# Performance work log

Hardware: AMD Instinct MI355X
Metric: run time of the kernel (lower is better)

The kernel has to match this reference:

```python
import jax, jax.numpy as jnp
import numpy as np

B, S, E, H = 2, 2048, 1024, 16
D = E // H  # head_dim = 64

def setup_inputs() -> dict:
    key = jax.random.key(0)
    ks = jax.random.split(key, 5)
    scale = 0.02
    return {
        "x": jax.random.normal(ks[0], (B, S, E), dtype=jnp.float32),
        "Wq": jax.random.normal(ks[1], (E, E), dtype=jnp.float32) * scale,
        "Wk": jax.random.normal(ks[2], (E, E), dtype=jnp.float32) * scale,
        "Wv": jax.random.normal(ks[3], (E, E), dtype=jnp.float32) * scale,
        "Wo": jax.random.normal(ks[4], (E, E), dtype=jnp.float32) * scale,
        "bo": jnp.zeros((E,), dtype=jnp.float32),
    }

def reference(x, Wq, Wk, Wv, Wo, bo):
    b, s, e = x.shape
    # Linear projections (torch Linear: x @ W.T), split heads -> (b, h, s, d)
    q = (x @ Wq.T).reshape(b, s, H, D).transpose(0, 2, 1, 3)
    k = (x @ Wk.T).reshape(b, s, H, D).transpose(0, 2, 1, 3)
    v = (x @ Wv.T).reshape(b, s, H, D).transpose(0, 2, 1, 3)
    # Full materialized causal scores (b, h, s, s)
    scores = jnp.einsum("bhqd,bhkd->bhqk", q, k)
    causal = jnp.tril(jnp.ones((s, s), dtype=bool))  # True = keep
    scores = jnp.where(causal, scores, -jnp.inf)
    attn = jax.nn.softmax(scores / jnp.sqrt(jnp.float32(D)), axis=-1)
    ctx = jnp.einsum("bhqk,bhkd->bhqd", attn, v)
    ctx = ctx.transpose(0, 2, 1, 3).reshape(b, s, e)
    return ctx @ Wo.T + bo
```

## Files before the change

### kernel.cpp

```cpp
#include <hip/hip_runtime.h>
#include <hip/hip_bf16.h>

typedef __attribute__((ext_vector_type(8))) short short8_t;
typedef __attribute__((ext_vector_type(4))) short s4v;
typedef __attribute__((ext_vector_type(4))) float f32x4_t;
using u16 = unsigned short;

constexpr int S_LEN = 2048;
constexpr int EMB   = 1024;
constexpr int NH    = 16;
constexpr int HD    = 64;
constexpr int BATCH = 2;
constexpr int MR    = BATCH * S_LEN;
constexpr int E3    = 3 * EMB;

#define L2E 1.44269504f

__device__ __forceinline__ u16 f2bf(float f) {
  unsigned u = __builtin_bit_cast(unsigned, f);
  unsigned r = 0x7fffu + ((u >> 16) & 1u);
  return (u16)((u + r) >> 16);
}

__device__ __forceinline__ void gld16(const void* g, void* l) {
  __builtin_amdgcn_global_load_lds(
      (const __attribute__((address_space(1))) void*)g,
      (__attribute__((address_space(3))) void*)l, 16, 0, 0);
}

template <int OFF>
__device__ __forceinline__ s4v tr16(const __attribute__((address_space(3))) u16* p) {
  s4v d;
  asm volatile("ds_read_b64_tr_b16 %0, %1 offset:%2"
               : "=v"(d) : "v"(p), "n"(OFF));
  return d;
}

__global__ void k_cvt_all(const float* __restrict__ x, const float* __restrict__ Wq,
                          const float* __restrict__ Wk, const float* __restrict__ Wv,
                          const float* __restrict__ Wo, u16* __restrict__ out) {
  int i = blockIdx.x * 256 + threadIdx.x;
  const float* src;
  int j;
  float sc = 1.0f;
  if (i < (1 << 20)) {
    src = x; j = i;
  } else {
    int jj = i - (1 << 20);
    int r = jj >> 18;
    j = jj & ((1 << 18) - 1);
    src = (r == 0) ? Wq : (r == 1) ? Wk : (r == 2) ? Wv : Wo;
    if (r == 0) sc = 0.125f;
  }
  float4 v = reinterpret_cast<const float4*>(src)[j];
  ushort4 o;
  o.x = f2bf(v.x * sc); o.y = f2bf(v.y * sc);
  o.z = f2bf(v.z * sc); o.w = f2bf(v.w * sc);
  reinterpret_cast<ushort4*>(out)[i] = o;
}

template <bool F32OUT>
__global__ __launch_bounds__(256) void k_gemm_bt(
    const u16* __restrict__ A, const u16* __restrict__ Bw,
    void* __restrict__ Cv, const float* __restrict__ bias,
    int M, int N, int K) {
  __shared__ short As[128 * 32];
  __shared__ short Bs[128 * 32];
  const int t    = threadIdx.x;
  const int w    = t >> 6;
  const int ln15 = t & 15;
  const int lg   = (t >> 4) & 3;
  const int wr   = w >> 1, wc = w & 1;
  const int m0   = blockIdx.y * 128, n0 = blockIdx.x * 128;

  const int srow = t >> 2;
  const int scol = (t & 3) * 8;
  const u16* gA = A + (size_t)(m0 + srow) * K + scol;
  const u16* gB = Bw + (size_t)(n0 + srow) * K + scol;
  short* lA = As + w * 512;
  short* lB = Bs + w * 512;

  f32x4_t acc[4][4] = {};

  for (int k0 = 0; k0 < K; k0 += 32) {
    gld16(gA + k0, lA);
    gld16(gA + (size_t)64 * K + k0, lA + 2048);
    gld16(gB + k0, lB);
    gld16(gB + (size_t)64 * K + k0, lB + 2048);
    __syncthreads();
    short8_t af[4], bf[4];
#pragma unroll
    for (int i = 0; i < 4; ++i) {
      af[i] = *reinterpret_cast<const short8_t*>(
          &As[(wr * 64 + i * 16 + ln15) * 32 + 8 * lg]);
      bf[i] = *reinterpret_cast<const short8_t*>(
          &Bs[(wc * 64 + i * 16 + ln15) * 32 + 8 * lg]);
    }
#pragma unroll
    for (int i = 0; i < 4; ++i)
#pragma unroll
      for (int j = 0; j < 4; ++j)
        acc[i][j] = __builtin_amdgcn_mfma_f32_16x16x32_bf16(
            af[i], bf[j], acc[i][j], 0, 0, 0);
    __syncthreads();
  }

  if (F32OUT) {
    float* C = reinterpret_cast<float*>(Cv);
#pragma unroll
    for (int i = 0; i < 4; ++i)
#pragma unroll
      for (int j = 0; j < 4; ++j) {
        const int col = n0 + wc * 64 + j * 16 + ln15;
        const float bv = bias ? bias[col] : 0.0f;
#pragma unroll
        for (int r = 0; r < 4; ++r) {
          const int row = m0 + wr * 64 + i * 16 + lg * 4 + r;
          C[(size_t)row * N + col] = acc[i][j][r] + bv;
        }
      }
  } else {
    u16* C = reinterpret_cast<u16*>(Cv);
#pragma unroll
    for (int i = 0; i < 4; ++i)
#pragma unroll
      for (int j = 0; j < 4; ++j) {
        const int col = n0 + wc * 64 + j * 16 + ln15;
#pragma unroll
        for (int r = 0; r < 4; ++r) {
          const int row = m0 + wr * 64 + i * 16 + lg * 4 + r;
          C[(size_t)row * N + col] = f2bf(acc[i][j][r]);
        }
      }
  }
}

__global__ __launch_bounds__(256, 4) void k_attn2(const u16* __restrict__ QKV,
                                                  u16* __restrict__ ctx) {
  __shared__ u16 Ks[2][64 * 64];
  __shared__ u16 Vs[2][64 * 64];

  const int t    = threadIdx.x;
  const int w    = t >> 6;
  const int l    = t & 63;
  const int ln15 = t & 15;
  const int lg   = (l >> 4) & 3;

  const int qt = 31 - blockIdx.y;
  const int bh = blockIdx.x;
  const int b  = bh >> 4, h = bh & 15;

  const u16* KVb = QKV + (size_t)b * S_LEN * E3 + h * HD;
  const u16* Kg  = KVb + 1024;
  const u16* Vg  = KVb + 2048;
  const int qrow = qt * 64 + w * 16;

  short8_t qf[2];
  {
    const u16* qp = KVb + (size_t)(qrow + ln15) * E3 + 8 * lg;
    qf[0] = *reinterpret_cast<const short8_t*>(qp);
    qf[1] = *reinterpret_cast<const short8_t*>(qp + 32);
  }

  const int krow_lo = l >> 3;
  const int kcol    = 8 * ((l & 7) ^ krow_lo);
  const int vkv     = l >> 1;
  const int vcol    = 16 * w + 8 * (l & 1);

  const int kx  = 8 * (ln15 & 7);
  const int kc0 = (8 * lg) ^ kx;
  const int kc1 = (32 + 8 * lg) ^ kx;

#define STAGE(buf, kv0)                                                        \
  do {                                                                         \
    gld16(Kg + (size_t)((kv0) + 16 * w + krow_lo) * E3 + kcol,                 \
          &Ks[buf][1024 * w]);                                                 \
    gld16(Kg + (size_t)((kv0) + 16 * w + 8 + krow_lo) * E3 + kcol,             \
          &Ks[buf][1024 * w + 512]);                                           \
    gld16(Vg + (size_t)((kv0) + vkv) * E3 + vcol, &Vs[buf][1024 * w]);         \
    gld16(Vg + (size_t)((kv0) + 32 + vkv) * E3 + vcol,                         \
          &Vs[buf][1024 * w + 512]);                                           \
  } while (0)

  f32x4_t o[4] = {};
  float mrow = -3e38f, lrow = 0.0f;
  const int nt_tiles = qt + 1;

  STAGE(0, 0);
  int cur = 0;

  for (int kvt = 0; kvt < nt_tiles; ++kvt) {
    const int kv0 = kvt * 64;
    asm volatile("s_barrier" ::: "memory");
    if (kvt + 1 < nt_tiles) {
      STAGE(cur ^ 1, kv0 + 64);
      asm volatile("s_waitcnt vmcnt(4)" ::: "memory");
    } else {
      asm volatile("s_waitcnt vmcnt(0)" ::: "memory");
    }
    asm volatile("s_barrier" ::: "memory");

    const __attribute__((address_space(3))) u16* vp =
        (const __attribute__((address_space(3))) u16*)&Vs[cur][4 * l];
    s4v vf[4][2][2];
#pragma unroll
    for (int nt = 0; nt < 4; ++nt) {
      if (nt == 0) { vf[0][0][0]=tr16<0>(vp);    vf[0][0][1]=tr16<512>(vp);
                     vf[0][1][0]=tr16<1024>(vp); vf[0][1][1]=tr16<1536>(vp); }
      if (nt == 1) { vf[1][0][0]=tr16<2048>(vp); vf[1][0][1]=tr16<2560>(vp);
                     vf[1][1][0]=tr16<3072>(vp); vf[1][1][1]=tr16<3584>(vp); }
      if (nt == 2) { vf[2][0][0]=tr16<4096>(vp); vf[2][0][1]=tr16<4608>(vp);
                     vf[2][1][0]=tr16<5120>(vp); vf[2][1][1]=tr16<5632>(vp); }
      if (nt == 3) { vf[3][0][0]=tr16<6144>(vp); vf[3][0][1]=tr16<6656>(vp);
                     vf[3][1][0]=tr16<7168>(vp); vf[3][1][1]=tr16<7680>(vp); }
    }

    f32x4_t tacc[4];
    __builtin_amdgcn_s_setprio(1);
#pragma unroll
    for (int ks = 0; ks < 4; ++ks) {
      const int R = 16 * ks + ln15;
      short8_t kf0 = *reinterpret_cast<const short8_t*>(&Ks[cur][R * 64 + kc0]);
      short8_t kf1 = *reinterpret_cast<const short8_t*>(&Ks[cur][R * 64 + kc1]);
      f32x4_t a = {0.f, 0.f, 0.f, 0.f};
      a = __builtin_amdgcn_mfma_f32_16x16x32_bf16(kf0, qf[0], a, 0, 0, 0);
      a = __builtin_amdgcn_mfma_f32_16x16x32_bf16(kf1, qf[1], a, 0, 0, 0);
      tacc[ks] = a;
    }
    __builtin_amdgcn_s_setprio(0);

    if (kvt == qt) {
      const int qg = qrow + ln15;
#pragma unroll
      for (int ks = 0; ks < 4; ++ks)
#pragma unroll
        for (int r = 0; r < 4; ++r)
          if (kv0 + 16 * ks + 4 * lg + r > qg) tacc[ks][r] = -3e38f;
    }

    float rm = fmaxf(
        fmaxf(fmaxf(fmaxf(tacc[0][0], tacc[0][1]), fmaxf(tacc[0][2], tacc[0][3])),
              fmaxf(fmaxf(tacc[1][0], tacc[1][1]), fmaxf(tacc[1][2], tacc[1][3]))),
        fmaxf(fmaxf(fmaxf(tacc[2][0], tacc[2][1]), fmaxf(tacc[2][2], tacc[2][3])),
              fmaxf(fmaxf(tacc[3][0], tacc[3][1]), fmaxf(tacc[3][2], tacc[3][3]))));
    rm = fmaxf(rm, __shfl_xor(rm, 16, 64));
    rm = fmaxf(rm, __shfl_xor(rm, 32, 64));

    if (__any(rm > mrow)) {
      const float nm = fmaxf(mrow, rm);
      const float sc = exp2f((mrow - nm) * L2E);
      mrow = nm;
      lrow *= sc;
#pragma unroll
      for (int r = 0; r < 4; ++r) {
        const float so = __shfl(sc, 20 * lg + r, 64);
#pragma unroll
        for (int nt = 0; nt < 4; ++nt) o[nt][r] *= so;
      }
    }

    const float nmL = mrow * L2E;
    float p[4][4];
    float rs = 0.0f;
#pragma unroll
    for (int ks = 0; ks < 4; ++ks)
#pragma unroll
      for (int r = 0; r < 4; ++r) {
        const float pv = exp2f(fmaf(tacc[ks][r], L2E, -nmL));
        p[ks][r] = pv;
        rs += pv;
      }
    rs += __shfl_xor(rs, 16, 64);
    rs += __shfl_xor(rs, 32, 64);
    lrow += rs;

    short8_t pf[2];
#pragma unroll
    for (int s2 = 0; s2 < 2; ++s2)
#pragma unroll
      for (int j = 0; j < 4; ++j) {
        pf[s2][j]     = (short)f2bf(p[2 * s2][j]);
        pf[s2][j + 4] = (short)f2bf(p[2 * s2 + 1][j]);
      }

    asm volatile("s_waitcnt lgkmcnt(0)");
    __builtin_amdgcn_sched_barrier(0);

    __builtin_amdgcn_s_setprio(1);
#pragma unroll
    for (int nt = 0; nt < 4; ++nt) {
#pragma unroll
      for (int s2 = 0; s2 < 2; ++s2) {
        short8_t bv = __builtin_shufflevector(vf[nt][s2][0], vf[nt][s2][1],
                                              0, 1, 2, 3, 4, 5, 6, 7);
        o[nt] = __builtin_amdgcn_mfma_f32_16x16x32_bf16(pf[s2], bv, o[nt], 0, 0, 0);
      }
    }
    __builtin_amdgcn_s_setprio(0);
    cur ^= 1;
  }
#undef STAGE

  const float linv = 1.0f / lrow;
#pragma unroll
  for (int r = 0; r < 4; ++r) {
    const float li = __shfl(linv, 20 * lg + r, 64);
    u16* op = ctx + (size_t)(b * S_LEN + qrow + 4 * lg + r) * EMB + h * HD;
#pragma unroll
    for (int nt = 0; nt < 4; ++nt)
      op[nt * 16 + ln15] = f2bf(o[nt][r] * li);
  }
}

extern "C" void kernel_launch(void* const* d_in, const int* in_sizes, int n_in,
                              void* d_out, int out_size, void* d_ws, size_t ws_size,
                              hipStream_t stream) {
  const float* x  = (const float*)d_in[0];
  const float* Wq = (const float*)d_in[1];
  const float* Wk = (const float*)d_in[2];
  const float* Wv = (const float*)d_in[3];
  const float* Wo = (const float*)d_in[4];
  const float* bo = (const float*)d_in[5];

  u16* ws   = (u16*)d_ws;
  u16* xb   = ws;
  u16* wcat = xb + (size_t)MR * EMB;
  u16* wob  = wcat + (size_t)3 * EMB * EMB;
  u16* qkv  = wob + (size_t)EMB * EMB;
  u16* ctxb = qkv + (size_t)MR * E3;

  k_cvt_all<<<8192, 256, 0, stream>>>(x, Wq, Wk, Wv, Wo, xb);

  k_gemm_bt<false><<<dim3(E3 / 128, MR / 128), 256, 0, stream>>>(
      xb, wcat, qkv, nullptr, MR, E3, EMB);

  k_attn2<<<dim3(BATCH * NH, 32), 256, 0, stream>>>(qkv, ctxb);

  k_gemm_bt<true><<<dim3(EMB / 128, MR / 128), 256, 0, stream>>>(
      ctxb, wob, d_out, bo, MR, EMB, EMB);
}
```

Before: 127.8 us.

## Process two 16-row query subtiles per wave in attention, halving block size

The attention kernel now launches 128 threads (2 waves) per 64-row query tile, with each wave handling 32 query rows as two 16-row subtiles instead of 16 rows. Each K fragment and V transposed fragment read from LDS is reused across two sets of MFMAs, which cuts LDS read traffic per FLOP. Staging is redistributed so each thread issues 8 global-to-LDS loads per tile. The cost is higher register pressure from doubled accumulators and softmax state, and half as many waves per block to hide latency.

```diff
diff --git a/kernel.cpp b/kernel.cpp
--- a/kernel.cpp
+++ b/kernel.cpp
@@ -135,7 +135,7 @@
   }
 }
 
-__global__ __launch_bounds__(256, 4) void k_attn2(const u16* __restrict__ QKV,
+__global__ __launch_bounds__(128, 2) void k_attn2(const u16* __restrict__ QKV,
                                                   u16* __restrict__ ctx) {
   __shared__ u16 Ks[2][64 * 64];
   __shared__ u16 Vs[2][64 * 64];
@@ -153,19 +153,20 @@
   const u16* KVb = QKV + (size_t)b * S_LEN * E3 + h * HD;
   const u16* Kg  = KVb + 1024;
   const u16* Vg  = KVb + 2048;
-  const int qrow = qt * 64 + w * 16;
-
-  short8_t qf[2];
-  {
-    const u16* qp = KVb + (size_t)(qrow + ln15) * E3 + 8 * lg;
-    qf[0] = *reinterpret_cast<const short8_t*>(qp);
-    qf[1] = *reinterpret_cast<const short8_t*>(qp + 32);
-  }
-
-  const int krow_lo = l >> 3;
-  const int kcol    = 8 * ((l & 7) ^ krow_lo);
-  const int vkv     = l >> 1;
-  const int vcol    = 16 * w + 8 * (l & 1);
+  const int qrow_w = qt * 64 + w * 32;
+
+  short8_t qf[2][2];
+#pragma unroll
+  for (int sub = 0; sub < 2; ++sub) {
+    const u16* qp = KVb + (size_t)(qrow_w + 16 * sub + ln15) * E3 + 8 * lg;
+    qf[sub][0] = *reinterpret_cast<const short8_t*>(qp);
+    qf[sub][1] = *reinterpret_cast<const short8_t*>(qp + 32);
+  }
+
+  const int krlo  = l >> 3;
+  const int kcsrc = 8 * ((l & 7) ^ krlo);
+  const int vkv   = l >> 1;
+  const int vdl   = 8 * (l & 1);
 
   const int kx  = 8 * (ln15 & 7);
   const int kc0 = (8 * lg) ^ kx;
@@ -173,17 +174,20 @@
 
 #define STAGE(buf, kv0)                                                        \
   do {                                                                         \
-    gld16(Kg + (size_t)((kv0) + 16 * w + krow_lo) * E3 + kcol,                 \
-          &Ks[buf][1024 * w]);                                                 \
-    gld16(Kg + (size_t)((kv0) + 16 * w + 8 + krow_lo) * E3 + kcol,             \
-          &Ks[buf][1024 * w + 512]);                                           \
-    gld16(Vg + (size_t)((kv0) + vkv) * E3 + vcol, &Vs[buf][1024 * w]);         \
-    gld16(Vg + (size_t)((kv0) + 32 + vkv) * E3 + vcol,                         \
-          &Vs[buf][1024 * w + 512]);                                           \
+    _Pragma("unroll")                                                          \
+    for (int i = 0; i < 4; ++i)                                                \
+      gld16(Kg + (size_t)((kv0) + 32 * w + 8 * i + krlo) * E3 + kcsrc,         \
+            &Ks[buf][w * 2048 + i * 512]);                                     \
+    _Pragma("unroll")                                                          \
+    for (int i = 0; i < 4; ++i) {                                              \
+      const int j = 4 * w + i;                                                 \
+      gld16(Vg + (size_t)((kv0) + 32 * (j & 1) + vkv) * E3 + 16 * (j >> 1) + vdl, \
+            &Vs[buf][j * 512]);                                                \
+    }                                                                          \
   } while (0)
 
-  f32x4_t o[4] = {};
-  float mrow = -3e38f, lrow = 0.0f;
+  f32x4_t o[2][4] = {};
+  float mrow[2] = {-3e38f, -3e38f}, lrow[2] = {0.0f, 0.0f};
   const int nt_tiles = qt + 1;
 
   STAGE(0, 0);
@@ -194,11 +198,28 @@
     asm volatile("s_barrier" ::: "memory");
     if (kvt + 1 < nt_tiles) {
       STAGE(cur ^ 1, kv0 + 64);
-      asm volatile("s_waitcnt vmcnt(4)" ::: "memory");
+      asm volatile("s_waitcnt vmcnt(8)" ::: "memory");
     } else {
       asm volatile("s_waitcnt vmcnt(0)" ::: "memory");
     }
     asm volatile("s_barrier" ::: "memory");
+
+    f32x4_t tacc[2][4];
+    __builtin_amdgcn_s_setprio(1);
+#pragma unroll
+    for (int ks = 0; ks < 4; ++ks) {
+      const int R = 16 * ks + ln15;
+      short8_t kf0 = *reinterpret_cast<const short8_t*>(&Ks[cur][R * 64 + kc0]);
+      short8_t kf1 = *reinterpret_cast<const short8_t*>(&Ks[cur][R * 64 + kc1]);
+#pragma unroll
+      for (int sub = 0; sub < 2; ++sub) {
+        f32x4_t a = {0.f, 0.f, 0.f, 0.f};
+        a = __builtin_amdgcn_mfma_f32_16x16x32_bf16(kf0, qf[sub][0], a, 0, 0, 0);
+        a = __builtin_amdgcn_mfma_f32_16x16x32_bf16(kf1, qf[sub][1], a, 0, 0, 0);
+        tacc[sub][ks] = a;
+      }
+    }
+    __builtin_amdgcn_s_setprio(0);
 
     const __attribute__((address_space(3))) u16* vp =
         (const __attribute__((address_space(3))) u16*)&Vs[cur][4 * l];
@@ -215,73 +236,75 @@
                      vf[3][1][0]=tr16<7168>(vp); vf[3][1][1]=tr16<7680>(vp); }
     }
 
-    f32x4_t tacc[4];
-    __builtin_amdgcn_s_setprio(1);
-#pragma unroll
-    for (int ks = 0; ks < 4; ++ks) {
-      const int R = 16 * ks + ln15;
-      short8_t kf0 = *reinterpret_cast<const short8_t*>(&Ks[cur][R * 64 + kc0]);
-      short8_t kf1 = *reinterpret_cast<const short8_t*>(&Ks[cur][R * 64 + kc1]);
-      f32x4_t a = {0.f, 0.f, 0.f, 0.f};
-      a = __builtin_amdgcn_mfma_f32_16x16x32_bf16(kf0, qf[0], a, 0, 0, 0);
-      a = __builtin_amdgcn_mfma_f32_16x16x32_bf16(kf1, qf[1], a, 0, 0, 0);
-      tacc[ks] = a;
-    }
-    __builtin_amdgcn_s_setprio(0);
-
     if (kvt == qt) {
-      const int qg = qrow + ln15;
+#pragma unroll
+      for (int sub = 0; sub < 2; ++sub) {
+        const int qg = qrow_w + 16 * sub + ln15;
+#pragma unroll
+        for (int ks = 0; ks < 4; ++ks)
+#pragma unroll
+          for (int r = 0; r < 4; ++r)
+            if (kv0 + 16 * ks + 4 * lg + r > qg) tacc[sub][ks][r] = -3e38f;
+      }
+    }
+
+    float rm[2];
+#pragma unroll
+    for (int sub = 0; sub < 2; ++sub) {
+      float m = fmaxf(
+          fmaxf(fmaxf(fmaxf(tacc[sub][0][0], tacc[sub][0][1]), fmaxf(tacc[sub][0][2], tacc[sub][0][3])),
+                fmaxf(fmaxf(tacc[sub][1][0], tacc[sub][1][1]), fmaxf(tacc[sub][1][2], tacc[sub][1][3]))),
+          fmaxf(fmaxf(fmaxf(tacc[sub][2][0], tacc[sub][2][1]), fmaxf(tacc[sub][2][2], tacc[sub][2][3])),
+                fmaxf(fmaxf(tacc[sub][3][0], tacc[sub][3][1]), fmaxf(tacc[sub][3][2], tacc[sub][3][3]))));
+      m = fmaxf(m, __shfl_xor(m, 16, 64));
+      m = fmaxf(m, __shfl_xor(m, 32, 64));
+      rm[sub] = m;
+    }
+
+    if (__any(fmaxf(rm[0] - mrow[0], rm[1] - mrow[1]) > 0.0f)) {
+#pragma unroll
+      for (int sub = 0; sub < 2; ++sub) {
+        const float nm = fmaxf(mrow[sub], rm[sub]);
+        const float sc = exp2f((mrow[sub] - nm) * L2E);
+        mrow[sub] = nm;
+        lrow[sub] *= sc;
+#pragma unroll
+        for (int r = 0; r < 4; ++r) {
+          const float so = __shfl(sc, 20 * lg + r, 64);
+#pragma unroll
+          for (int nt = 0; nt < 4; ++nt) o[sub][nt][r] *= so;
+        }
+      }
+    }
+
+    float p[2][4][4];
+#pragma unroll
+    for (int sub = 0; sub < 2; ++sub) {
+      const float nmL = mrow[sub] * L2E;
+      float rs = 0.0f;
 #pragma unroll
       for (int ks = 0; ks < 4; ++ks)
 #pragma unroll
-        for (int r = 0; r < 4; ++r)
-          if (kv0 + 16 * ks + 4 * lg + r > qg) tacc[ks][r] = -3e38f;
-    }
-
-    float rm = fmaxf(
-        fmaxf(fmaxf(fmaxf(tacc[0][0], tacc[0][1]), fmaxf(tacc[0][2], tacc[0][3])),
-              fmaxf(fmaxf(tacc[1][0], tacc[1][1]), fmaxf(tacc[1][2], tacc[1][3]))),
-        fmaxf(fmaxf(fmaxf(tacc[2][0], tacc[2][1]), fmaxf(tacc[2][2], tacc[2][3])),
-              fmaxf(fmaxf(tacc[3][0], tacc[3][1]), fmaxf(tacc[3][2], tacc[3][3]))));
-    rm = fmaxf(rm, __shfl_xor(rm, 16, 64));
-    rm = fmaxf(rm, __shfl_xor(rm, 32, 64));
-
-    if (__any(rm > mrow)) {
-      const float nm = fmaxf(mrow, rm);
-      const float sc = exp2f((mrow - nm) * L2E);
-      mrow = nm;
-      lrow *= sc;
-#pragma unroll
-      for (int r = 0; r < 4; ++r) {
-        const float so = __shfl(sc, 20 * lg + r, 64);
-#pragma unroll
-        for (int nt = 0; nt < 4; ++nt) o[nt][r] *= so;
-      }
-    }
-
-    const float nmL = mrow * L2E;
-    float p[4][4];
-    float rs = 0.0f;
-#pragma unroll
-    for (int ks = 0; ks < 4; ++ks)
-#pragma unroll
-      for (int r = 0; r < 4; ++r) {
-        const float pv = exp2f(fmaf(tacc[ks][r], L2E, -nmL));
-        p[ks][r] = pv;
-        rs += pv;
-      }
-    rs += __shfl_xor(rs, 16, 64);
-    rs += __shfl_xor(rs, 32, 64);
-    lrow += rs;
-
-    short8_t pf[2];
-#pragma unroll
-    for (int s2 = 0; s2 < 2; ++s2)
-#pragma unroll
-      for (int j = 0; j < 4; ++j) {
-        pf[s2][j]     = (short)f2bf(p[2 * s2][j]);
-        pf[s2][j + 4] = (short)f2bf(p[2 * s2 + 1][j]);
-      }
+        for (int r = 0; r < 4; ++r) {
+          const float pv = exp2f(fmaf(tacc[sub][ks][r], L2E, -nmL));
+          p[sub][ks][r] = pv;
+          rs += pv;
+        }
+      rs += __shfl_xor(rs, 16, 64);
+      rs += __shfl_xor(rs, 32, 64);
+      lrow[sub] += rs;
+    }
+
+    short8_t pf[2][2];
+#pragma unroll
+    for (int sub = 0; sub < 2; ++sub)
+#pragma unroll
+      for (int s2 = 0; s2 < 2; ++s2)
+#pragma unroll
+        for (int j = 0; j < 4; ++j) {
+          pf[sub][s2][j]     = (short)f2bf(p[sub][2 * s2][j]);
+          pf[sub][s2][j + 4] = (short)f2bf(p[sub][2 * s2 + 1][j]);
+        }
 
     asm volatile("s_waitcnt lgkmcnt(0)");
     __builtin_amdgcn_sched_barrier(0);
@@ -293,7 +316,8 @@
       for (int s2 = 0; s2 < 2; ++s2) {
         short8_t bv = __builtin_shufflevector(vf[nt][s2][0], vf[nt][s2][1],
                                               0, 1, 2, 3, 4, 5, 6, 7);
-        o[nt] = __builtin_amdgcn_mfma_f32_16x16x32_bf16(pf[s2], bv, o[nt], 0, 0, 0);
+        o[0][nt] = __builtin_amdgcn_mfma_f32_16x16x32_bf16(pf[0][s2], bv, o[0][nt], 0, 0, 0);
+        o[1][nt] = __builtin_amdgcn_mfma_f32_16x16x32_bf16(pf[1][s2], bv, o[1][nt], 0, 0, 0);
       }
     }
     __builtin_amdgcn_s_setprio(0);
@@ -301,14 +325,17 @@
   }
 #undef STAGE
 
-  const float linv = 1.0f / lrow;
-#pragma unroll
-  for (int r = 0; r < 4; ++r) {
-    const float li = __shfl(linv, 20 * lg + r, 64);
-    u16* op = ctx + (size_t)(b * S_LEN + qrow + 4 * lg + r) * EMB + h * HD;
-#pragma unroll
-    for (int nt = 0; nt < 4; ++nt)
-      op[nt * 16 + ln15] = f2bf(o[nt][r] * li);
+#pragma unroll
+  for (int sub = 0; sub < 2; ++sub) {
+    const float linv = 1.0f / lrow[sub];
+#pragma unroll
+    for (int r = 0; r < 4; ++r) {
+      const float li = __shfl(linv, 20 * lg + r, 64);
+      u16* op = ctx + (size_t)(b * S_LEN + qrow_w + 16 * sub + 4 * lg + r) * EMB + h * HD;
+#pragma unroll
+      for (int nt = 0; nt < 4; ++nt)
+        op[nt * 16 + ln15] = f2bf(o[sub][nt][r] * li);
+    }
   }
 }
 
@@ -334,7 +361,7 @@
   k_gemm_bt<false><<<dim3(E3 / 128, MR / 128), 256, 0, stream>>>(
       xb, wcat, qkv, nullptr, MR, E3, EMB);
 
-  k_attn2<<<dim3(BATCH * NH, 32), 256, 0, stream>>>(qkv, ctxb);
+  k_attn2<<<dim3(BATCH * NH, 32), 128, 0, stream>>>(qkv, ctxb);
 
   k_gemm_bt<true><<<dim3(EMB / 128, MR / 128), 256, 0, stream>>>(
       ctxb, wob, d_out, bo, MR, EMB, EMB);
```

After: 151.6 us. 18.6% more time.
